# Optimization experiments

Measured on AMD Instinct MI355X. Metric: run time of the kernel, lower is better.

Reference implementation:

```python
import jax, jax.numpy as jnp
import numpy as np

BITS = 4
N_PACK = 32 // BITS  # int32 compression
GROUPSIZE = 128
MASK = (1 << BITS) - 1


def _unpack_int32(q, axis):
    """Unpack int32 tensor into N_PACK low-bit values along `axis`.
    Element j*N_PACK+e comes from bits [BITS*e, BITS*(e+1)) of packed word j."""
    parts = [ (q >> (BITS * e)) & MASK for e in range(N_PACK) ]
    u = jnp.stack(parts, axis=axis + 1)  # (..., P, N_PACK, ...)
    shape = list(q.shape)
    shape[axis] = shape[axis] * N_PACK
    return u.reshape(shape)


def setup_inputs() -> dict:
    key = jax.random.key(0)
    k1, k2, k3, k4, k5 = jax.random.split(key, 5)
    in_f, out_f = 4096, 12288
    tokens = 8192
    n_groups = in_f // GROUPSIZE  # 32
    x = jax.random.normal(k1, (tokens, in_f), dtype=jnp.float32)
    scales = jax.random.uniform(k2, (n_groups, out_f), dtype=jnp.float32) * 0.01 + 1e-3
    bias = jax.random.normal(k3, (out_f,), dtype=jnp.float32)
    qweight = jax.random.randint(k4, (in_f // N_PACK, out_f), jnp.iinfo(jnp.int32).min, jnp.iinfo(jnp.int32).max, dtype=jnp.int32)
    qzeros = jax.random.randint(k5, (n_groups, out_f // N_PACK), jnp.iinfo(jnp.int32).min, jnp.iinfo(jnp.int32).max, dtype=jnp.int32)
    return {"x": x, "scales": scales, "bias": bias, "qweight": qweight, "qzeros": qzeros}


def reference(x, scales, bias, qweight, qzeros):
    in_f = qweight.shape[0] * N_PACK
    out_f = qweight.shape[1]
    n_groups = scales.shape[0]
    # Unpack 4-bit weights along input-channel axis: (in_f, out_f), values 0..15
    w_int = _unpack_int32(qweight, axis=0).astype(scales.dtype)
    # Unpack zero points along output-channel axis; optimum format stores zp-1
    zp = (_unpack_int32(qzeros, axis=1) + 1).astype(scales.dtype)  # (n_groups, out_f)
    # Per-group dequant: group g covers input channels [g*GROUPSIZE, (g+1)*GROUPSIZE)
    w = (w_int.reshape(n_groups, GROUPSIZE, out_f) - zp[:, None, :]) * scales[:, None, :]
    w = w.reshape(in_f, out_f)
    # Linear: y = x @ W^T with W = w.T, i.e. x @ w
    return x @ w + bias
```

## Files before the change

kernel.cpp:

```cpp
#include <hip/hip_runtime.h>
#include <hip/hip_bf16.h>


typedef __attribute__((ext_vector_type(8))) short short8;
typedef __attribute__((ext_vector_type(4))) float f32x4;

__device__ __forceinline__ short f2bf(float f) {
  unsigned u = __float_as_uint(f);
  u += 0x7fffu + ((u >> 16) & 1u);
  return (short)(u >> 16);
}

__device__ __forceinline__ void gload_lds16(const void* g, void* l) {
  __builtin_amdgcn_global_load_lds(
      (const __attribute__((address_space(1))) void*)g,
      (__attribute__((address_space(3))) void*)l,
      16, 0, 0);
}

__device__ __forceinline__ void bar() {
  asm volatile("" ::: "memory");
  __builtin_amdgcn_s_barrier();
  asm volatile("" ::: "memory");
}
__device__ __forceinline__ void wait_vm3() {
  asm volatile("s_waitcnt vmcnt(3)" ::: "memory");
}
__device__ __forceinline__ void wait_vm0() {
  asm volatile("s_waitcnt vmcnt(0)" ::: "memory");
}

__global__ __launch_bounds__(256) void dequant_tile_kernel(
    const int* __restrict__ qweight, const int* __restrict__ qzeros,
    const float* __restrict__ scales, short* __restrict__ Bt,
    int N, int K) {
  const int ktn = K >> 5;
  const int bx = blockIdx.x;
  const int nb = bx / ktn, kt = bx - nb * ktn;
  const int t = threadIdx.x;
  const int g = kt >> 2;
  char* dst = (char*)Bt + (size_t)bx * 8192;
#pragma unroll
  for (int p = 0; p < 2; ++p) {
    const int c = p * 256 + t;
    const int l = c & 63;
    const int n = nb * 128 + (c >> 6) * 16 + (l & 15);
    const int kw = kt * 4 + (l >> 4);
    const float sc = scales[(size_t)g * N + n];
    const int zw = qzeros[(size_t)g * (N >> 3) + (n >> 3)];
    const float zs = -(float)(((zw >> ((n & 7) * 4)) & 15) + 1) * sc;
    const int w = qweight[(size_t)kw * N + n];
    short8 v;
#pragma unroll
    for (int e = 0; e < 8; ++e)
      v[e] = f2bf(fmaf((float)((w >> (4 * e)) & 15), sc, zs));
    *(short8*)(dst + c * 16) = v;
  }
}

__global__ __launch_bounds__(256) void cvt_tile_kernel(
    const float* __restrict__ x, short* __restrict__ xb, int K) {
  const int ktn = K >> 5;
  const int bx = blockIdx.x;
  const int mb = bx / ktn, kt = bx - mb * ktn;
  char* dst = (char*)xb + (size_t)bx * 16384;
#pragma unroll
  for (int p = 0; p < 4; ++p) {
    const int c = p * 256 + threadIdx.x;
    const int l = c & 63;
    const int row = mb * 256 + (c >> 6) * 16 + (l & 15);
    const int k = kt * 32 + (l >> 4) * 8;
    const float* s = x + (size_t)row * K + k;
    float4 f0 = *(const float4*)s;
    float4 f1 = *(const float4*)(s + 4);
    short8 v;
    v[0] = f2bf(f0.x); v[1] = f2bf(f0.y); v[2] = f2bf(f0.z); v[3] = f2bf(f0.w);
    v[4] = f2bf(f1.x); v[5] = f2bf(f1.y); v[6] = f2bf(f1.z); v[7] = f2bf(f1.w);
    *(short8*)(dst + c * 16) = v;
  }
}

#define GBM 256
#define GBN 128

__global__ __launch_bounds__(512, 4) void gemm256_kernel(
    const short* __restrict__ At, const short* __restrict__ Bt,
    const float* __restrict__ bias, float* __restrict__ C,
    int M, int N, int K) {
  __shared__ __align__(16) char lds[3 * 24576];
  const int tid = threadIdx.x;
  const int nbx = N / GBN;
  const int nwg = gridDim.x;
  int bid = blockIdx.x;
  if ((nwg & 7) == 0) bid = (bid & 7) * (nwg >> 3) + (bid >> 3);
  const int mb = bid / nbx;
  const int nb = bid % nbx;
  const int bm = mb * GBM, bn = nb * GBN;

  const int wid = tid >> 6, lane = tid & 63;
  const int wr = wid >> 1, wc = wid & 1;

  const int P = K >> 5;

  char* lb = &lds[0];

  const char* aBase = lb + wr * 4096 + lane * 16;
  const char* bBase = lb + 16384 + wc * 4096 + lane * 16;

  const char* pA = (const char*)At + (size_t)mb * P * 16384 + (size_t)tid * 16;
  const char* pB = (const char*)Bt + (size_t)nb * P * 8192 + (size_t)tid * 16;
  char* dA = lb + tid * 16;
  char* dB = lb + 16384 + tid * 16;

#define STAGE(TSL, AOFF, BOFF)                                \
  do {                                                        \
    gload_lds16(pA + (AOFF), dA + (TSL)*24576);               \
    gload_lds16(pA + (AOFF) + 8192, dA + (TSL)*24576 + 8192); \
    gload_lds16(pB + (BOFF), dB + (TSL)*24576);               \
  } while (0)

  short8 aR[4], bR[4];

#define RD(SL)                                                        \
  do {                                                                \
    _Pragma("unroll") for (int i = 0; i < 4; ++i) aR[i] =             \
        *(const short8*)(aBase + (SL)*24576 + i * 1024);              \
    _Pragma("unroll") for (int j = 0; j < 4; ++j) bR[j] =             \
        *(const short8*)(bBase + (SL)*24576 + j * 1024);              \
  } while (0)

  f32x4 acc[4][4] = {};

#define MFMA16()                                                         \
  do {                                                                   \
    __builtin_amdgcn_s_setprio(1);                                       \
    _Pragma("unroll") for (int i = 0; i < 4; ++i)                        \
        _Pragma("unroll") for (int j = 0; j < 4; ++j) acc[i][j] =        \
            __builtin_amdgcn_mfma_f32_16x16x32_bf16(aR[i], bR[j],        \
                                                    acc[i][j], 0, 0, 0); \
    __builtin_amdgcn_s_setprio(0);                                       \
  } while (0)

  STAGE(0, 0, 0);
  STAGE(1, 16384, 8192);

  const int nIt = (P - 2) / 3;
  for (int it = 0; it < nIt; ++it) {
    wait_vm3(); bar();
    RD(0); STAGE(2, 2 * 16384, 2 * 8192); MFMA16();
    wait_vm3(); bar();
    RD(1); STAGE(0, 3 * 16384, 3 * 8192); MFMA16();
    wait_vm3(); bar();
    RD(2); STAGE(1, 4 * 16384, 4 * 8192); MFMA16();
    pA += 3 * 16384;
    pB += 3 * 8192;
  }
  wait_vm3(); bar();
  RD(0); MFMA16();
  wait_vm0(); bar();
  RD(1); MFMA16();

#undef MFMA16
#undef RD
#undef STAGE

  const int crow0 = bm + wr * 64 + (lane >> 4) * 4;
  const int ccol0 = bn + wc * 64 + (lane & 15);
#pragma unroll
  for (int fj = 0; fj < 4; ++fj) {
    const float bv = bias[ccol0 + fj * 16];
#pragma unroll
    for (int fi = 0; fi < 4; ++fi) {
#pragma unroll
      for (int r = 0; r < 4; ++r) {
        C[(size_t)(crow0 + fi * 16 + r) * N + ccol0 + fj * 16] =
            acc[fi][fj][r] + bv;
      }
    }
  }
}

__global__ __launch_bounds__(256) void dequant_kernel(
    const int* __restrict__ qweight, const int* __restrict__ qzeros,
    const float* __restrict__ scales, short* __restrict__ Wt,
    int in_f, int out_f) {
  __shared__ __align__(16) short T[64][72];
  const int n0 = blockIdx.x * 64;
  const int k0 = blockIdx.y * 64;
  const int t = threadIdx.x;
  const int nl = t & 63;
  const int kw = t >> 6;
  const int n = n0 + nl;
  const int g = k0 >> 7;
  const float sc = scales[(size_t)g * out_f + n];
  const int zpw = qzeros[(size_t)g * (out_f >> 3) + (n >> 3)];
  const float zp = (float)(((zpw >> ((n & 7) * 4)) & 15) + 1);
  const float zs = zp * sc;
#pragma unroll
  for (int rr = 0; rr < 2; ++rr) {
    const int kwi = kw + rr * 4;
    const int w = qweight[(size_t)((k0 >> 3) + kwi) * out_f + n];
    short8 v;
#pragma unroll
    for (int e = 0; e < 8; ++e) {
      float f = (float)((w >> (4 * e)) & 15) * sc - zs;
      v[e] = f2bf(f);
    }
    *(short8*)&T[nl][kwi * 8] = v;
  }
  __syncthreads();
#pragma unroll
  for (int rr = 0; rr < 2; ++rr) {
    const int c = rr * 256 + t;
    const int row = c >> 3, ch = c & 7;
    *(short8*)&Wt[(size_t)(n0 + row) * in_f + k0 + ch * 8] =
        *(const short8*)&T[row][ch * 8];
  }
}

__global__ __launch_bounds__(256) void cvt_kernel(
    const float* __restrict__ x, short* __restrict__ xb, long n8) {
  long i = (long)blockIdx.x * blockDim.x + threadIdx.x;
  if (i >= n8) return;
  const float* src = x + i * 8;
  float4 a = *(const float4*)src;
  float4 b = *(const float4*)(src + 4);
  short8 v;
  v[0] = f2bf(a.x); v[1] = f2bf(a.y); v[2] = f2bf(a.z); v[3] = f2bf(a.w);
  v[4] = f2bf(b.x); v[5] = f2bf(b.y); v[6] = f2bf(b.z); v[7] = f2bf(b.w);
  *(short8*)(xb + i * 8) = v;
}

#define BM 128
#define BN 128
#define BK 64

template <bool A_BF16>
__global__ __launch_bounds__(256) void gemm_bias_kernel(
    const void* __restrict__ Av, const short* __restrict__ Bt,
    const float* __restrict__ bias, float* __restrict__ C,
    int M, int N, int K) {
  __shared__ __align__(16) short As[BM * BK];
  __shared__ __align__(16) short Bs[BN * BK];
  const int tid = threadIdx.x;
  const int bm = blockIdx.y * BM;
  const int bn = blockIdx.x * BN;
  const int wid = tid >> 6, lane = tid & 63;
  const int wr = wid >> 1, wc = wid & 1;
  const int lrow = lane & 15;
  const int lk = (lane >> 4) * 8;

  f32x4 acc[4][4] = {};

  for (int kt = 0; kt < K; kt += BK) {
    if constexpr (A_BF16) {
      const short* A = (const short*)Av;
#pragma unroll
      for (int r = 0; r < 4; ++r) {
        const int c = r * 256 + tid;
        const int row = c >> 3, ch = c & 7;
        gload_lds16(A + (size_t)(bm + row) * K + kt + ch * 8,
                    (char*)As + c * 16);
      }
    } else {
      const float* A = (const float*)Av;
#pragma unroll
      for (int r = 0; r < 4; ++r) {
        const int c = r * 256 + tid;
        const int row = c >> 3, ch = c & 7;
        const float* src = A + (size_t)(bm + row) * K + kt + ch * 8;
        float4 f0 = *(const float4*)src;
        float4 f1 = *(const float4*)(src + 4);
        short8 v;
        v[0] = f2bf(f0.x); v[1] = f2bf(f0.y); v[2] = f2bf(f0.z); v[3] = f2bf(f0.w);
        v[4] = f2bf(f1.x); v[5] = f2bf(f1.y); v[6] = f2bf(f1.z); v[7] = f2bf(f1.w);
        *(short8*)((char*)As + c * 16) = v;
      }
    }
#pragma unroll
    for (int r = 0; r < 4; ++r) {
      const int c = r * 256 + tid;
      const int row = c >> 3, ch = c & 7;
      gload_lds16(Bt + (size_t)(bn + row) * K + kt + ch * 8,
                  (char*)Bs + c * 16);
    }
    __syncthreads();
#pragma unroll
    for (int kk = 0; kk < 2; ++kk) {
      short8 af[4], bf[4];
#pragma unroll
      for (int i = 0; i < 4; ++i)
        af[i] = *(const short8*)&As[(wr * 64 + i * 16 + lrow) * BK + kk * 32 + lk];
#pragma unroll
      for (int j = 0; j < 4; ++j)
        bf[j] = *(const short8*)&Bs[(wc * 64 + j * 16 + lrow) * BK + kk * 32 + lk];
#pragma unroll
      for (int i = 0; i < 4; ++i)
#pragma unroll
        for (int j = 0; j < 4; ++j)
          acc[i][j] = __builtin_amdgcn_mfma_f32_16x16x32_bf16(
              af[i], bf[j], acc[i][j], 0, 0, 0);
    }
    __syncthreads();
  }

  const int crow0 = bm + wr * 64 + (lane >> 4) * 4;
  const int ccol0 = bn + wc * 64 + (lane & 15);
#pragma unroll
  for (int j = 0; j < 4; ++j) {
    const float bv = bias[ccol0 + j * 16];
#pragma unroll
    for (int i = 0; i < 4; ++i) {
#pragma unroll
      for (int r = 0; r < 4; ++r) {
        C[(size_t)(crow0 + i * 16 + r) * N + ccol0 + j * 16] = acc[i][j][r] + bv;
      }
    }
  }
}

__global__ __launch_bounds__(256) void naive_kernel(
    const float* __restrict__ x, const float* __restrict__ scales,
    const float* __restrict__ bias, const int* __restrict__ qw,
    const int* __restrict__ qz, float* __restrict__ out,
    int M, int K, int N) {
  long idx = (long)blockIdx.x * blockDim.x + threadIdx.x;
  if (idx >= (long)M * N) return;
  const int n = (int)(idx % N);
  const int m = (int)(idx / N);
  float acc = 0.f;
  for (int g = 0; g < K / 128; ++g) {
    const float sc = scales[(size_t)g * N + n];
    const float zp =
        (float)(((qz[(size_t)g * (N >> 3) + (n >> 3)] >> ((n & 7) * 4)) & 15) + 1);
    const float zs = zp * sc;
    for (int kw = 0; kw < 16; ++kw) {
      const int w = qw[(size_t)(g * 16 + kw) * N + n];
      const float* xp = &x[(size_t)m * K + g * 128 + kw * 8];
#pragma unroll
      for (int e = 0; e < 8; ++e)
        acc += xp[e] * ((float)((w >> (4 * e)) & 15) * sc - zs);
    }
  }
  out[idx] = acc + bias[n];
}

extern "C" void kernel_launch(void* const* d_in, const int* in_sizes, int n_in,
                              void* d_out, int out_size, void* d_ws,
                              size_t ws_size, hipStream_t stream) {
  const float* x = (const float*)d_in[0];
  const float* scales = (const float*)d_in[1];
  const float* bias = (const float*)d_in[2];
  const int* qweight = (const int*)d_in[3];
  const int* qzeros = (const int*)d_in[4];
  float* out = (float*)d_out;

  const int out_f = in_sizes[2];
  const int kwords = in_sizes[3] / out_f;
  const int in_f = kwords * 8;
  const int tokens = in_sizes[0] / in_f;
  const int M = tokens, K = in_f, N = out_f;

  const size_t wt_bytes = (size_t)K * N * sizeof(short);
  const size_t xb_bytes = (size_t)M * K * sizeof(short);

  const bool div128 = (M % BM == 0) && (N % BN == 0) && (K % BK == 0) &&
                      (K % 128 == 0) && (N % 64 == 0);
  const bool divR18 = (M % GBM == 0) && (N % GBN == 0) && (K % 256 == 0) &&
                      (((K >> 5) - 2) % 3 == 0);

  if (divR18 && ws_size >= wt_bytes + xb_bytes) {
    short* Btile = (short*)d_ws;
    short* Atile = (short*)((char*)d_ws + wt_bytes);
    const int ktn = K >> 5;
    dequant_tile_kernel<<<(N / 128) * ktn, 256, 0, stream>>>(
        qweight, qzeros, scales, Btile, N, K);
    cvt_tile_kernel<<<(M / 256) * ktn, 256, 0, stream>>>(x, Atile, K);
    gemm256_kernel<<<(M / GBM) * (N / GBN), 512, 0, stream>>>(
        Atile, Btile, bias, out, M, N, K);
  } else if (div128 && ws_size >= wt_bytes + xb_bytes) {
    short* Wt = (short*)d_ws;
    short* xb = (short*)((char*)d_ws + wt_bytes);
    dequant_kernel<<<dim3(N / 64, K / 64), 256, 0, stream>>>(
        qweight, qzeros, scales, Wt, K, N);
    const long n8 = (long)M * K / 8;
    cvt_kernel<<<(int)((n8 + 255) / 256), 256, 0, stream>>>(x, xb, n8);
    gemm_bias_kernel<true><<<dim3(N / BN, M / BM), 256, 0, stream>>>(
        xb, Wt, bias, out, M, N, K);
  } else if (div128 && ws_size >= wt_bytes) {
    short* Wt = (short*)d_ws;
    dequant_kernel<<<dim3(N / 64, K / 64), 256, 0, stream>>>(
        qweight, qzeros, scales, Wt, K, N);
    gemm_bias_kernel<false><<<dim3(N / BN, M / BM), 256, 0, stream>>>(
        x, Wt, bias, out, M, N, K);
  } else {
    const long total = (long)M * N;
    naive_kernel<<<(int)((total + 255) / 256), 256, 0, stream>>>(
        x, scales, bias, qweight, qzeros, out, M, K, N);
  }
}
```

Measured before the change: 751.1 us.

## Load GEMM B operand straight into registers, keeping only A in LDS

The B tile no longer goes through LDS. Each wave now loads its 64-column B fragment directly from global memory into a double-buffered register set, tracked with explicit vmcnt waits. LDS per block drops from three 24KB slots to three 16KB A slots, and the main loop is unrolled six-fold so the B register sets alternate cleanly. This cuts LDS traffic and footprint, which may allow more resident blocks. In exchange, the four waves sharing a column half each fetch the same B data from global/L2, and register pressure goes up.

```diff
diff --git a/kernel.cpp b/kernel.cpp
--- a/kernel.cpp
+++ b/kernel.cpp
@@ -22,12 +22,6 @@
   asm volatile("" ::: "memory");
   __builtin_amdgcn_s_barrier();
   asm volatile("" ::: "memory");
-}
-__device__ __forceinline__ void wait_vm3() {
-  asm volatile("s_waitcnt vmcnt(3)" ::: "memory");
-}
-__device__ __forceinline__ void wait_vm0() {
-  asm volatile("s_waitcnt vmcnt(0)" ::: "memory");
 }
 
 __global__ __launch_bounds__(256) void dequant_tile_kernel(
@@ -87,7 +81,7 @@
     const short* __restrict__ At, const short* __restrict__ Bt,
     const float* __restrict__ bias, float* __restrict__ C,
     int M, int N, int K) {
-  __shared__ __align__(16) char lds[3 * 24576];
+  __shared__ __align__(16) char lds[3 * 16384];
   const int tid = threadIdx.x;
   const int nbx = N / GBN;
   const int nwg = gridDim.x;
@@ -105,63 +99,98 @@
   char* lb = &lds[0];
 
   const char* aBase = lb + wr * 4096 + lane * 16;
-  const char* bBase = lb + 16384 + wc * 4096 + lane * 16;
 
   const char* pA = (const char*)At + (size_t)mb * P * 16384 + (size_t)tid * 16;
-  const char* pB = (const char*)Bt + (size_t)nb * P * 8192 + (size_t)tid * 16;
   char* dA = lb + tid * 16;
-  char* dB = lb + 16384 + tid * 16;
-
-#define STAGE(TSL, AOFF, BOFF)                                \
-  do {                                                        \
-    gload_lds16(pA + (AOFF), dA + (TSL)*24576);               \
-    gload_lds16(pA + (AOFF) + 8192, dA + (TSL)*24576 + 8192); \
-    gload_lds16(pB + (BOFF), dB + (TSL)*24576);               \
+
+  const char* pB = (const char*)Bt + (size_t)nb * P * 8192 + wc * 4096 +
+                   (size_t)lane * 16;
+
+  short8 bs[2][4];
+
+#define STAGE(TSL, AOFF)                                 \
+  do {                                                   \
+    gload_lds16(pA + (AOFF), dA + (TSL)*16384);          \
+    gload_lds16(pA + (AOFF) + 8192, dA + (TSL)*16384 + 8192); \
   } while (0)
 
-  short8 aR[4], bR[4];
-
-#define RD(SL)                                                        \
-  do {                                                                \
-    _Pragma("unroll") for (int i = 0; i < 4; ++i) aR[i] =             \
-        *(const short8*)(aBase + (SL)*24576 + i * 1024);              \
-    _Pragma("unroll") for (int j = 0; j < 4; ++j) bR[j] =             \
-        *(const short8*)(bBase + (SL)*24576 + j * 1024);              \
+#define LOADB(SET, BOFF)                                             \
+  do {                                                               \
+    asm volatile("global_load_dwordx4 %0, %1, off"                   \
+                 : "=v"(bs[SET][0]) : "v"(pB + (BOFF)));             \
+    asm volatile("global_load_dwordx4 %0, %1, off"                   \
+                 : "=v"(bs[SET][1]) : "v"(pB + (BOFF) + 1024));      \
+    asm volatile("global_load_dwordx4 %0, %1, off"                   \
+                 : "=v"(bs[SET][2]) : "v"(pB + (BOFF) + 2048));      \
+    asm volatile("global_load_dwordx4 %0, %1, off"                   \
+                 : "=v"(bs[SET][3]) : "v"(pB + (BOFF) + 3072));      \
   } while (0)
 
+#define WAITB(NSTR, SET)                                                   \
+  asm volatile("s_waitcnt vmcnt(" NSTR ")"                                 \
+               : "+v"(bs[SET][0]), "+v"(bs[SET][1]), "+v"(bs[SET][2]),     \
+                 "+v"(bs[SET][3])::"memory")
+
+  short8 aR[4];
+
+#define RDA(SL)                                                   \
+  do {                                                            \
+    _Pragma("unroll") for (int i = 0; i < 4; ++i) aR[i] =         \
+        *(const short8*)(aBase + (SL)*16384 + i * 1024);          \
+  } while (0)
+
   f32x4 acc[4][4] = {};
 
-#define MFMA16()                                                         \
+#define MFMA16(SET)                                                      \
   do {                                                                   \
     __builtin_amdgcn_s_setprio(1);                                       \
     _Pragma("unroll") for (int i = 0; i < 4; ++i)                        \
         _Pragma("unroll") for (int j = 0; j < 4; ++j) acc[i][j] =        \
-            __builtin_amdgcn_mfma_f32_16x16x32_bf16(aR[i], bR[j],        \
+            __builtin_amdgcn_mfma_f32_16x16x32_bf16(aR[i], bs[SET][j],   \
                                                     acc[i][j], 0, 0, 0); \
     __builtin_amdgcn_s_setprio(0);                                       \
   } while (0)
 
-  STAGE(0, 0, 0);
-  STAGE(1, 16384, 8192);
-
-  const int nIt = (P - 2) / 3;
+#define PHASE(SL, SET, R)                                  \
+  do {                                                     \
+    WAITB("2", SET);                                       \
+    bar();                                                 \
+    RDA(SL);                                               \
+    LOADB((SET) ^ 1, ((R) + 1) * 8192);                    \
+    STAGE(((SL) + 2) % 3, ((R) + 2) * 16384);              \
+    MFMA16(SET);                                           \
+  } while (0)
+
+  STAGE(0, 0);
+  LOADB(0, 0);
+  STAGE(1, 16384);
+
+  const int nIt = (P - 2) / 6;
   for (int it = 0; it < nIt; ++it) {
-    wait_vm3(); bar();
-    RD(0); STAGE(2, 2 * 16384, 2 * 8192); MFMA16();
-    wait_vm3(); bar();
-    RD(1); STAGE(0, 3 * 16384, 3 * 8192); MFMA16();
-    wait_vm3(); bar();
-    RD(2); STAGE(1, 4 * 16384, 4 * 8192); MFMA16();
-    pA += 3 * 16384;
-    pB += 3 * 8192;
-  }
-  wait_vm3(); bar();
-  RD(0); MFMA16();
-  wait_vm0(); bar();
-  RD(1); MFMA16();
-
+    PHASE(0, 0, 0);
+    PHASE(1, 1, 1);
+    PHASE(2, 0, 2);
+    PHASE(0, 1, 3);
+    PHASE(1, 0, 4);
+    PHASE(2, 1, 5);
+    pA += 6 * 16384;
+    pB += 6 * 8192;
+  }
+  WAITB("2", 0);
+  bar();
+  RDA(0);
+  LOADB(1, 1 * 8192);
+  MFMA16(0);
+  WAITB("0", 1);
+  bar();
+  RDA(1);
+  MFMA16(1);
+
+#undef PHASE
 #undef MFMA16
-#undef RD
+#undef RDA
+#undef WAITB
+#undef LOADB
 #undef STAGE
 
   const int crow0 = bm + wr * 64 + (lane >> 4) * 4;
@@ -366,10 +395,10 @@
 
   const bool div128 = (M % BM == 0) && (N % BN == 0) && (K % BK == 0) &&
                       (K % 128 == 0) && (N % 64 == 0);
-  const bool divR18 = (M % GBM == 0) && (N % GBN == 0) && (K % 256 == 0) &&
-                      (((K >> 5) - 2) % 3 == 0);
-
-  if (divR18 && ws_size >= wt_bytes + xb_bytes) {
+  const bool divR19 = (M % GBM == 0) && (N % GBN == 0) && (K % 256 == 0) &&
+                      (((K >> 5) - 2) % 6 == 0);
+
+  if (divR19 && ws_size >= wt_bytes + xb_bytes) {
     short* Btile = (short*)d_ws;
     short* Atile = (short*)((char*)d_ws + wt_bytes);
     const int ktn = K >> 5;
```

Result: slower. 887.0 us (+18.1%).
